# Kernel optimization log

Hardware: AMD Instinct MI355X
Metric: run time of the kernel (lower is better)

## Reference

```python
import jax, jax.numpy as jnp
import numpy as np

N, E, NFEAT, H = 100000, 1600000, 128, 128
NLAYER = 3


def setup_inputs() -> dict:
    key = jax.random.key(0)
    ks = jax.random.split(key, 20)
    s = 0.05
    return {
        "features": jax.random.normal(ks[0], (N, NFEAT), jnp.float32),
        "edge_index": jax.random.randint(ks[1], (2, E), 0, N, jnp.int32),
        "edge_weight": jax.random.uniform(ks[2], (E,), jnp.float32),
        "w1": jax.random.normal(ks[3], (H, NFEAT), jnp.float32) * s,
        "b1": jnp.zeros((H,), jnp.float32),
        "gin_w1": jax.random.normal(ks[4], (NLAYER, H, H), jnp.float32) * s,
        "gin_b1": jnp.zeros((NLAYER, H), jnp.float32),
        "gin_w2": jax.random.normal(ks[5], (NLAYER, H, H), jnp.float32) * s,
        "gin_b2": jnp.zeros((NLAYER, H), jnp.float32),
        "gru_wih": jax.random.normal(ks[6], (NLAYER, 3 * H, H), jnp.float32) * s,
        "gru_whh": jax.random.normal(ks[7], (NLAYER, 3 * H, H), jnp.float32) * s,
        "gru_bih": jnp.zeros((NLAYER, 3 * H), jnp.float32),
        "gru_bhh": jnp.zeros((NLAYER, 3 * H), jnp.float32),
        "head_w1": jax.random.normal(ks[8], (NLAYER, H, H), jnp.float32) * s,
        "head_b1": jnp.zeros((NLAYER, H), jnp.float32),
        "head_w2_0": jax.random.normal(ks[9], (2, H), jnp.float32) * s,
        "head_b2_0": jnp.zeros((2,), jnp.float32),
        "head_w2_1": jax.random.normal(ks[10], (6, H), jnp.float32) * s,
        "head_b2_1": jnp.zeros((6,), jnp.float32),
        "head_w2_2": jax.random.normal(ks[11], (21, H), jnp.float32) * s,
        "head_b2_2": jnp.zeros((21,), jnp.float32),
    }


def _gru_cell(x, h, wih, whh, bih, bhh):
    # torch.nn.GRUCell semantics
    gi = x @ wih.T + bih           # [N, 3H]
    gh = h @ whh.T + bhh           # [N, 3H]
    ir, iz, inn = jnp.split(gi, 3, axis=1)
    hr, hz, hn = jnp.split(gh, 3, axis=1)
    r = jax.nn.sigmoid(ir + hr)
    z = jax.nn.sigmoid(iz + hz)
    n = jnp.tanh(inn + r * hn)
    return (1.0 - z) * n + z * h


def reference(features, edge_index, edge_weight, w1, b1,
              gin_w1, gin_b1, gin_w2, gin_b2,
              gru_wih, gru_whh, gru_bih, gru_bhh,
              head_w1, head_b1,
              head_w2_0, head_b2_0, head_w2_1, head_b2_1, head_w2_2, head_b2_2):
    n_nodes = features.shape[0]
    dst, src = edge_index[0], edge_index[1]  # spmm: out[dst] += w * x[src]
    head_w2 = [head_w2_0, head_w2_1, head_w2_2]
    head_b2 = [head_b2_0, head_b2_1, head_b2_2]

    x = jax.nn.relu(features @ w1.T + b1)  # mlp1 + ReLU
    layer_info = x
    outputs, _outputs = [], []
    for i in range(NLAYER):
        agg = jax.ops.segment_sum(edge_weight[:, None] * x[src], dst,
                                  num_segments=n_nodes)
        h = _gru_cell(agg, layer_info, gru_wih[i], gru_whh[i],
                      gru_bih[i], gru_bhh[i])
        # GinMlp: Linear -> ReLU -> Linear, then outer ReLU
        x = jax.nn.relu(h @ gin_w1[i].T + gin_b1[i]) @ gin_w2[i].T + gin_b2[i]
        x = jax.nn.relu(x)
        # custom layer-norm variant
        x = x / jnp.sqrt(1.0 + jnp.sum(x * x, axis=1, keepdims=True))
        # prediction head for this layer (mlpPos = [0,1,2])
        tmp = jax.nn.relu(x @ head_w1[i].T + head_b1[i]) @ head_w2[i].T + head_b2[i]
        outputs.append(jax.nn.log_softmax(tmp, axis=1))
        _outputs.append(jax.nn.softmax(tmp, axis=1))
        layer_info = x
    return tuple(outputs) + tuple(_outputs)
```

## Files before the change

kernel.cpp:

```cpp
#include <hip/hip_runtime.h>
#include <cstdint>
#include <cstddef>


typedef short  v8s __attribute__((ext_vector_type(8)));
typedef float  v4f __attribute__((ext_vector_type(4)));

#define BUCKET_CAP 4096

static __device__ __forceinline__ float bf2f(uint16_t u) {
  return __uint_as_float(((uint32_t)u) << 16);
}
static __device__ __forceinline__ uint16_t f2b(float f) {
  uint32_t x = __float_as_uint(f);
  return (uint16_t)((x + 0x7FFFu + ((x >> 16) & 1u)) >> 16);
}
static __device__ __forceinline__ float sigmoidf_(float v) {
  return 1.f / (1.f + __expf(-v));
}
static __device__ __forceinline__ float tanhf_(float v) {
  return 1.f - 2.f / (__expf(2.f * v) + 1.f);
}

__global__ void k_detect(const uint32_t* __restrict__ u, int* __restrict__ flag) {
  int lane = threadIdx.x;
  uint32_t low = u[lane] & 0xFFFFu;
  uint32_t e = (low >> 7) & 0xFFu;
  bool pass = (e == 0) || (e >= 110 && e <= 141);
  unsigned long long b = __ballot(pass);
  if (lane == 0) *flag = (__popcll(b) >= 32) ? 1 : 0;
}

struct CvtDesc {
  const void* src[18];
  int off[19];
};

__global__ void k_cvtw(CvtDesc c, float* __restrict__ wbase,
                       uint16_t* __restrict__ wb16,
                       const int* __restrict__ flag, int total) {
  int gid = blockIdx.x * 256 + threadIdx.x;
  if (gid >= total) return;
  int t = 0;
#pragma unroll
  for (int i = 1; i < 18; i++)
    if (gid >= c.off[i]) t = i;
  int local = gid - c.off[t];
  float v;
  if (*flag) v = bf2f(((const uint16_t*)c.src[t])[local]);
  else       v = ((const float*)c.src[t])[local];
  wbase[gid] = v;
  wb16[gid] = f2b(v);
}

__global__ void k_cvt_feat(const void* __restrict__ src, uint16_t* __restrict__ dst,
                           int n, const int* __restrict__ flag) {
  int i = blockIdx.x * 256 + threadIdx.x;
  if (i >= n) return;
  if (*flag) dst[i] = ((const uint16_t*)src)[i];
  else       dst[i] = f2b(((const float*)src)[i]);
}

__global__ void k_zero_i(int* __restrict__ p, int n) {
  int i = blockIdx.x * 256 + threadIdx.x;
  if (i < n) p[i] = 0;
}

__global__ void k_zero_f(float* __restrict__ p, int n) {
  int i = blockIdx.x * 256 + threadIdx.x;
  if (i < n) p[i] = 0.f;
}

__global__ void k_pack_mm(const uint16_t* __restrict__ src, uint16_t* __restrict__ dst,
                          int nmat) {
  int id = blockIdx.x * 256 + threadIdx.x;
  if (id >= nmat * 2048) return;
  int mat = id >> 11;
  int rem = id & 2047;
  int blk = rem >> 6, lane = rem & 63;
  int kc = blk >> 3, t = blk & 7;
  int n0 = lane & 15, quad = lane >> 4;
  const uint16_t* s = src + (size_t)mat * 16384 + (size_t)(t * 16 + n0) * 128 + kc * 32 + quad * 8;
  uint16_t* d = dst + (size_t)id * 8;
  *reinterpret_cast<v8s*>(d) = *reinterpret_cast<const v8s*>(s);
}

__global__ void k_pack_gru(const uint16_t* __restrict__ wih, const uint16_t* __restrict__ whh,
                           uint16_t* __restrict__ dst, int nlayer) {
  int id = blockIdx.x * 256 + threadIdx.x;
  if (id >= nlayer * 192 * 64) return;
  int lane = id & 63;
  int blk = (id >> 6) % 192;
  int layer = (id >> 6) / 192;
  int g = blk % 3;
  int mat = (blk / 3) % 2;
  int u = (blk / 6) % 2;
  int w = (blk / 12) % 4;
  int kc = blk / 48;
  int n0 = lane & 15, quad = lane >> 4;
  const uint16_t* base = (mat == 0 ? wih : whh) + (size_t)layer * 384 * 128;
  const uint16_t* s = base + (size_t)(g * 128 + w * 32 + u * 16 + n0) * 128 + kc * 32 + quad * 8;
  uint16_t* d = dst + ((size_t)layer * 192 + blk) * 512 + (size_t)lane * 8;
  *reinterpret_cast<v8s*>(d) = *reinterpret_cast<const v8s*>(s);
}

__global__ void k_part(const int* __restrict__ dst, const int* __restrict__ src,
                       const void* __restrict__ w, int* __restrict__ gcur,
                       uint2* __restrict__ ep0, const int* __restrict__ flag,
                       int E, int NB) {
  __shared__ int hist[1024];
  __shared__ int lbase[1024];
  int t = threadIdx.x;
  int CH = (E + gridDim.x - 1) / gridDim.x;
  int e0 = blockIdx.x * CH;
  int e1 = e0 + CH;
  if (e1 > E) e1 = E;
  for (int b = t; b < NB; b += 256) hist[b] = 0;
  __syncthreads();
  for (int e = e0 + t; e < e1; e += 256)
    atomicAdd(&hist[dst[e] >> 7], 1);
  __syncthreads();
  for (int b = t; b < NB; b += 256) {
    int c = hist[b];
    lbase[b] = c ? atomicAdd(&gcur[b], c) : 0;
    hist[b] = 0;
  }
  __syncthreads();
  bool bf = (*flag) != 0;
  for (int e = e0 + t; e < e1; e += 256) {
    int d = dst[e];
    int b = d >> 7;
    int pos = lbase[b] + atomicAdd(&hist[b], 1);
    if (pos >= BUCKET_CAP) pos = BUCKET_CAP - 1;
    float wv = bf ? bf2f(((const uint16_t*)w)[e]) : ((const float*)w)[e];
    ep0[(size_t)b * BUCKET_CAP + pos] =
        make_uint2((uint32_t)src[e] | (((uint32_t)d & 127u) << 25),
                   __float_as_uint(wv));
  }
}

__global__ void k_bprefix(const int* __restrict__ gcur, int* __restrict__ bbase,
                          int nbuckets) {
  __shared__ int red[256];
  int t = threadIdx.x;
  int chunk = (nbuckets + 255) >> 8;
  int beg = t * chunk;
  int end = beg + chunk;
  if (end > nbuckets) end = nbuckets;
  int s = 0;
  for (int b = beg; b < end; b++) {
    int c = gcur[b];
    if (c > BUCKET_CAP) c = BUCKET_CAP;
    bbase[b] = c;
    s += c;
  }
  red[t] = s;
  __syncthreads();
  for (int off = 1; off < 256; off <<= 1) {
    int u = (t >= off) ? red[t - off] : 0;
    __syncthreads();
    red[t] += u;
    __syncthreads();
  }
  int run = red[t] - s;
  for (int b = beg; b < end; b++) {
    int tot = bbase[b];
    bbase[b] = run;
    run += tot;
  }
}

__global__ void k_build(const uint2* __restrict__ ep0, const int* __restrict__ gcur,
                        const int* __restrict__ bbase, int* __restrict__ rowptr,
                        uint2* __restrict__ ep, int n, int nbuckets) {
  __shared__ int lcnt[128];
  __shared__ int lsc[128];
  int b = blockIdx.x, t = threadIdx.x;
  int cnt = gcur[b];
  if (cnt > BUCKET_CAP) cnt = BUCKET_CAP;
  if (t < 128) lcnt[t] = 0;
  __syncthreads();

  const uint2* sp = ep0 + (size_t)b * BUCKET_CAP;
  for (int p = t; p < cnt; p += 256)
    atomicAdd(&lcnt[sp[p].x >> 25], 1);
  __syncthreads();

  if (t < 128) lsc[t] = lcnt[t];
  __syncthreads();
  for (int off = 1; off < 128; off <<= 1) {
    int v = 0;
    if (t < 128 && t >= off) v = lsc[t - off];
    __syncthreads();
    if (t < 128) lsc[t] += v;
    __syncthreads();
  }

  int base = bbase[b];
  if (t < 128) {
    int excl = lsc[t] - lcnt[t];
    int node = b * 128 + t;
    if (node < n) rowptr[node] = base + excl;
    lcnt[t] = base + excl;
  }
  if (b == nbuckets - 1 && t == 0) rowptr[n] = base + lsc[127];
  __syncthreads();

  for (int p = t; p < cnt; p += 256) {
    uint2 v = sp[p];
    int pos = atomicAdd(&lcnt[v.x >> 25], 1);
    ep[pos] = make_uint2(v.x & 0x01FFFFFFu, v.y);
  }
}

__global__ void k_spmm(const uint16_t* __restrict__ x, const int* __restrict__ rowptr,
                       const uint2* __restrict__ ep, uint16_t* __restrict__ agg, int n) {
  int node = blockIdx.x * 4 + (threadIdx.x >> 6);
  int lane = threadIdx.x & 63;
  if (node >= n) return;
  int p0 = rowptr[node], p1 = rowptr[node + 1];
  float a0 = 0.f, a1 = 0.f;
  const uint16_t* xc = x + (size_t)lane * 2;
  int p = p0;
  for (; p + 7 < p1; p += 8) {
    uint2 e0 = ep[p], e1 = ep[p + 1], e2 = ep[p + 2], e3 = ep[p + 3];
    uint2 e4 = ep[p + 4], e5 = ep[p + 5], e6 = ep[p + 6], e7 = ep[p + 7];
    uint32_t u0 = *reinterpret_cast<const uint32_t*>(xc + (size_t)e0.x * 128);
    uint32_t u1 = *reinterpret_cast<const uint32_t*>(xc + (size_t)e1.x * 128);
    uint32_t u2 = *reinterpret_cast<const uint32_t*>(xc + (size_t)e2.x * 128);
    uint32_t u3 = *reinterpret_cast<const uint32_t*>(xc + (size_t)e3.x * 128);
    uint32_t u4 = *reinterpret_cast<const uint32_t*>(xc + (size_t)e4.x * 128);
    uint32_t u5 = *reinterpret_cast<const uint32_t*>(xc + (size_t)e5.x * 128);
    uint32_t u6 = *reinterpret_cast<const uint32_t*>(xc + (size_t)e6.x * 128);
    uint32_t u7 = *reinterpret_cast<const uint32_t*>(xc + (size_t)e7.x * 128);
    float w0 = __uint_as_float(e0.y), w1 = __uint_as_float(e1.y);
    float w2 = __uint_as_float(e2.y), w3 = __uint_as_float(e3.y);
    float w4 = __uint_as_float(e4.y), w5 = __uint_as_float(e5.y);
    float w6 = __uint_as_float(e6.y), w7 = __uint_as_float(e7.y);
    a0 = fmaf(w0, bf2f((uint16_t)u0), a0);
    a1 = fmaf(w0, bf2f((uint16_t)(u0 >> 16)), a1);
    a0 = fmaf(w1, bf2f((uint16_t)u1), a0);
    a1 = fmaf(w1, bf2f((uint16_t)(u1 >> 16)), a1);
    a0 = fmaf(w2, bf2f((uint16_t)u2), a0);
    a1 = fmaf(w2, bf2f((uint16_t)(u2 >> 16)), a1);
    a0 = fmaf(w3, bf2f((uint16_t)u3), a0);
    a1 = fmaf(w3, bf2f((uint16_t)(u3 >> 16)), a1);
    a0 = fmaf(w4, bf2f((uint16_t)u4), a0);
    a1 = fmaf(w4, bf2f((uint16_t)(u4 >> 16)), a1);
    a0 = fmaf(w5, bf2f((uint16_t)u5), a0);
    a1 = fmaf(w5, bf2f((uint16_t)(u5 >> 16)), a1);
    a0 = fmaf(w6, bf2f((uint16_t)u6), a0);
    a1 = fmaf(w6, bf2f((uint16_t)(u6 >> 16)), a1);
    a0 = fmaf(w7, bf2f((uint16_t)u7), a0);
    a1 = fmaf(w7, bf2f((uint16_t)(u7 >> 16)), a1);
  }
  for (; p + 1 < p1; p += 2) {
    uint2 e0 = ep[p], e1 = ep[p + 1];
    uint32_t u0 = *reinterpret_cast<const uint32_t*>(xc + (size_t)e0.x * 128);
    uint32_t u1 = *reinterpret_cast<const uint32_t*>(xc + (size_t)e1.x * 128);
    float w0 = __uint_as_float(e0.y), w1 = __uint_as_float(e1.y);
    a0 = fmaf(w0, bf2f((uint16_t)u0), a0);
    a1 = fmaf(w0, bf2f((uint16_t)(u0 >> 16)), a1);
    a0 = fmaf(w1, bf2f((uint16_t)u1), a0);
    a1 = fmaf(w1, bf2f((uint16_t)(u1 >> 16)), a1);
  }
  for (; p < p1; p++) {
    uint2 e0 = ep[p];
    float w0 = __uint_as_float(e0.y);
    uint32_t u0 = *reinterpret_cast<const uint32_t*>(xc + (size_t)e0.x * 128);
    a0 = fmaf(w0, bf2f((uint16_t)u0), a0);
    a1 = fmaf(w0, bf2f((uint16_t)(u0 >> 16)), a1);
  }
  uint32_t packed = (uint32_t)f2b(a0) | ((uint32_t)f2b(a1) << 16);
  *reinterpret_cast<uint32_t*>(agg + (size_t)node * 128 + lane * 2) = packed;
}

template <int EPI>
__launch_bounds__(256)
__global__ void k_mm(const uint16_t* __restrict__ A, const uint16_t* __restrict__ Wrp,
                     const float* __restrict__ bias, uint16_t* __restrict__ C,
                     int nrows) {
  int wave = threadIdx.x >> 6, lane = threadIdx.x & 63;
  int n0 = lane & 15, quad = lane >> 4;
  int m0 = (blockIdx.x * 4 + wave) * 32;
  int r0 = m0 + n0, r1 = m0 + 16 + n0;
  bool ok0 = r0 < nrows, ok1 = r1 < nrows;
  const v8s z8 = {0, 0, 0, 0, 0, 0, 0, 0};

  v4f acc[2][8];
#pragma unroll
  for (int rt = 0; rt < 2; rt++)
#pragma unroll
    for (int t = 0; t < 8; t++) acc[rt][t] = {0.f, 0.f, 0.f, 0.f};

  const uint16_t* ap0 = A + (size_t)r0 * 128 + quad * 8;
  const uint16_t* ap1 = A + (size_t)r1 * 128 + quad * 8;
#pragma unroll
  for (int kc = 0; kc < 4; kc++) {
    v8s a0 = ok0 ? *reinterpret_cast<const v8s*>(ap0 + kc * 32) : z8;
    v8s a1 = ok1 ? *reinterpret_cast<const v8s*>(ap1 + kc * 32) : z8;
    const uint16_t* wp = Wrp + (size_t)kc * 4096 + (size_t)lane * 8;
#pragma unroll
    for (int t = 0; t < 8; t++) {
      v8s bf = *reinterpret_cast<const v8s*>(wp + t * 512);
      acc[0][t] = __builtin_amdgcn_mfma_f32_16x16x32_bf16(a0, bf, acc[0][t], 0, 0, 0);
      acc[1][t] = __builtin_amdgcn_mfma_f32_16x16x32_bf16(a1, bf, acc[1][t], 0, 0, 0);
    }
  }

#pragma unroll
  for (int rt = 0; rt < 2; rt++) {
    int mb = m0 + rt * 16;
    float vv[8][4];
#pragma unroll
    for (int t = 0; t < 8; t++) {
      float b = bias[t * 16 + n0];
#pragma unroll
      for (int r = 0; r < 4; r++) vv[t][r] = fmaxf(acc[rt][t][r] + b, 0.f);
    }
    if (EPI == 2) {
#pragma unroll
      for (int r = 0; r < 4; r++) {
        float ss = 0.f;
#pragma unroll
        for (int t = 0; t < 8; t++) ss = fmaf(vv[t][r], vv[t][r], ss);
        ss += __shfl_xor(ss, 1);
        ss += __shfl_xor(ss, 2);
        ss += __shfl_xor(ss, 4);
        ss += __shfl_xor(ss, 8);
        float sc = rsqrtf(1.f + ss);
#pragma unroll
        for (int t = 0; t < 8; t++) vv[t][r] *= sc;
      }
    }
#pragma unroll
    for (int r = 0; r < 4; r++) {
      int row = mb + quad * 4 + r;
      if (row >= nrows) continue;
#pragma unroll
      for (int t = 0; t < 8; t++)
        C[(size_t)row * 128 + t * 16 + n0] = f2b(vv[t][r]);
    }
  }
}

template <int C>
__launch_bounds__(256)
__global__ void k_mm12h(const uint16_t* __restrict__ A,
                        const uint16_t* __restrict__ W1rp, const float* __restrict__ b1,
                        const uint16_t* __restrict__ W2rp, const float* __restrict__ b2,
                        const uint16_t* __restrict__ Whrp, const float* __restrict__ bh,
                        const float* __restrict__ w2, const float* __restrict__ b2h,
                        uint16_t* __restrict__ xbout,
                        float* __restrict__ out_log, float* __restrict__ out_soft,
                        int nrows) {
  __shared__ uint16_t hl[64][136];
  int wave = threadIdx.x >> 6, lane = threadIdx.x & 63;
  int n0 = lane & 15, quad = lane >> 4;
  int m0 = blockIdx.x * 64 + wave * 16;
  int r0 = m0 + n0;
  bool ok0 = r0 < nrows;
  const v8s z8 = {0, 0, 0, 0, 0, 0, 0, 0};

  v4f acc[8];
#pragma unroll
  for (int t = 0; t < 8; t++) acc[t] = {0.f, 0.f, 0.f, 0.f};

  const uint16_t* ap0 = A + (size_t)r0 * 128 + quad * 8;
#pragma unroll
  for (int kc = 0; kc < 4; kc++) {
    v8s a0 = ok0 ? *reinterpret_cast<const v8s*>(ap0 + kc * 32) : z8;
    const uint16_t* wp = W1rp + (size_t)kc * 4096 + (size_t)lane * 8;
#pragma unroll
    for (int t = 0; t < 8; t++) {
      v8s bf = *reinterpret_cast<const v8s*>(wp + t * 512);
      acc[t] = __builtin_amdgcn_mfma_f32_16x16x32_bf16(a0, bf, acc[t], 0, 0, 0);
    }
  }
#pragma unroll
  for (int t = 0; t < 8; t++) {
    float b = b1[t * 16 + n0];
#pragma unroll
    for (int r = 0; r < 4; r++) {
      int rl = wave * 16 + quad * 4 + r;
      hl[rl][t * 16 + n0] = f2b(fmaxf(acc[t][r] + b, 0.f));
    }
  }
  __syncthreads();

  v4f acc2[8];
#pragma unroll
  for (int t = 0; t < 8; t++) acc2[t] = {0.f, 0.f, 0.f, 0.f};
#pragma unroll
  for (int kc = 0; kc < 4; kc++) {
    v8s a0 = *reinterpret_cast<const v8s*>(&hl[wave * 16 + n0][kc * 32 + quad * 8]);
    const uint16_t* wp = W2rp + (size_t)kc * 4096 + (size_t)lane * 8;
#pragma unroll
    for (int t = 0; t < 8; t++) {
      v8s bf = *reinterpret_cast<const v8s*>(wp + t * 512);
      acc2[t] = __builtin_amdgcn_mfma_f32_16x16x32_bf16(a0, bf, acc2[t], 0, 0, 0);
    }
  }
  __syncthreads();
  {
    float vv[8][4];
#pragma unroll
    for (int t = 0; t < 8; t++) {
      float b = b2[t * 16 + n0];
#pragma unroll
      for (int r = 0; r < 4; r++) vv[t][r] = fmaxf(acc2[t][r] + b, 0.f);
    }
#pragma unroll
    for (int r = 0; r < 4; r++) {
      float ss = 0.f;
#pragma unroll
      for (int t = 0; t < 8; t++) ss = fmaf(vv[t][r], vv[t][r], ss);
      ss += __shfl_xor(ss, 1);
      ss += __shfl_xor(ss, 2);
      ss += __shfl_xor(ss, 4);
      ss += __shfl_xor(ss, 8);
      float sc = rsqrtf(1.f + ss);
#pragma unroll
      for (int t = 0; t < 8; t++) vv[t][r] *= sc;
    }
#pragma unroll
    for (int r = 0; r < 4; r++) {
      int row = m0 + quad * 4 + r;
      int rl = wave * 16 + quad * 4 + r;
#pragma unroll
      for (int t = 0; t < 8; t++) {
        uint16_t hv = f2b(vv[t][r]);
        hl[rl][t * 16 + n0] = hv;
        if (row < nrows) xbout[(size_t)row * 128 + t * 16 + n0] = hv;
      }
    }
  }
  __syncthreads();

  v4f acc3[8];
#pragma unroll
  for (int t = 0; t < 8; t++) acc3[t] = {0.f, 0.f, 0.f, 0.f};
#pragma unroll
  for (int kc = 0; kc < 4; kc++) {
    v8s a0 = *reinterpret_cast<const v8s*>(&hl[wave * 16 + n0][kc * 32 + quad * 8]);
    const uint16_t* wp = Whrp + (size_t)kc * 4096 + (size_t)lane * 8;
#pragma unroll
    for (int t = 0; t < 8; t++) {
      v8s bf = *reinterpret_cast<const v8s*>(wp + t * 512);
      acc3[t] = __builtin_amdgcn_mfma_f32_16x16x32_bf16(a0, bf, acc3[t], 0, 0, 0);
    }
  }
  __syncthreads();
#pragma unroll
  for (int t = 0; t < 8; t++) {
    float b = bh[t * 16 + n0];
#pragma unroll
    for (int r = 0; r < 4; r++) {
      int rl = wave * 16 + quad * 4 + r;
      hl[rl][t * 16 + n0] = f2b(fmaxf(acc3[t][r] + b, 0.f));
    }
  }
  __syncthreads();

  {
    int row = threadIdx.x >> 2;
    int s = threadIdx.x & 3;
    int node = blockIdx.x * 64 + row;
    float lg[C];
#pragma unroll
    for (int c = 0; c < C; c++) lg[c] = 0.f;
    const uint32_t* hr = reinterpret_cast<const uint32_t*>(&hl[row][0]);
#pragma unroll
    for (int j = 0; j < 16; j++) {
      uint32_t u = hr[j * 4 + s];
      float x0 = bf2f((uint16_t)u);
      float x1 = bf2f((uint16_t)(u >> 16));
      int k0 = 2 * (j * 4 + s);
#pragma unroll
      for (int c = 0; c < C; c++) lg[c] = fmaf(x0, w2[c * 128 + k0], lg[c]);
#pragma unroll
      for (int c = 0; c < C; c++) lg[c] = fmaf(x1, w2[c * 128 + k0 + 1], lg[c]);
    }
#pragma unroll
    for (int c = 0; c < C; c++) {
      lg[c] += __shfl_xor(lg[c], 1);
      lg[c] += __shfl_xor(lg[c], 2);
    }
    if (s == 0 && node < nrows) {
#pragma unroll
      for (int c = 0; c < C; c++) lg[c] += b2h[c];
      float m = lg[0];
#pragma unroll
      for (int c = 1; c < C; c++) m = fmaxf(m, lg[c]);
      float sum = 0.f;
      float e[C];
#pragma unroll
      for (int c = 0; c < C; c++) { e[c] = __expf(lg[c] - m); sum += e[c]; }
      float ls = __logf(sum);
      float inv = 1.f / sum;
#pragma unroll
      for (int c = 0; c < C; c++) {
        out_log[(size_t)node * C + c] = lg[c] - m - ls;
        out_soft[(size_t)node * C + c] = e[c] * inv;
      }
    }
  }
}

__launch_bounds__(512, 2)
__global__ void k_gru8(const uint16_t* __restrict__ agg, const uint16_t* __restrict__ xb,
                       const uint16_t* __restrict__ Wrp,
                       const float* __restrict__ bih, const float* __restrict__ bhh,
                       uint16_t* __restrict__ hb, int n, int ntiles) {
  int wave = threadIdx.x >> 6, lane = threadIdx.x & 63;
  int n0 = lane & 15, quad = lane >> 4;
  int s = wave >> 1, u = wave & 1;
  const v8s z8 = {0, 0, 0, 0, 0, 0, 0, 0};

  v8s wf[24];
#pragma unroll
  for (int kc = 0; kc < 4; kc++)
#pragma unroll
    for (int mat = 0; mat < 2; mat++)
#pragma unroll
      for (int g = 0; g < 3; g++)
        wf[kc * 6 + mat * 3 + g] = *reinterpret_cast<const v8s*>(
            Wrp + (size_t)((kc * 4 + s) * 12 + (u * 2 + mat) * 3 + g) * 512 +
            (size_t)lane * 8);

  int col = wave * 16 + n0;
  float bir = bih[col], biz = bih[128 + col], bin = bih[256 + col];
  float bhr = bhh[col], bhz = bhh[128 + col], bhn = bhh[256 + col];

  for (int tt = blockIdx.x; tt < ntiles; tt += gridDim.x) {
    int m0 = tt * 32;
    int r0 = m0 + n0, r1 = m0 + 16 + n0;
    bool ok0 = r0 < n, ok1 = r1 < n;

    v4f accI[2][3], accH[2][3];
#pragma unroll
    for (int rt = 0; rt < 2; rt++)
#pragma unroll
      for (int g = 0; g < 3; g++) {
        accI[rt][g] = {0.f, 0.f, 0.f, 0.f};
        accH[rt][g] = {0.f, 0.f, 0.f, 0.f};
      }

    const uint16_t* ap0 = agg + (size_t)r0 * 128 + quad * 8;
    const uint16_t* ap1 = agg + (size_t)r1 * 128 + quad * 8;
    const uint16_t* xp0 = xb + (size_t)r0 * 128 + quad * 8;
    const uint16_t* xp1 = xb + (size_t)r1 * 128 + quad * 8;
#pragma unroll
    for (int kc = 0; kc < 4; kc++) {
      v8s a0 = ok0 ? *reinterpret_cast<const v8s*>(ap0 + kc * 32) : z8;
      v8s a1 = ok1 ? *reinterpret_cast<const v8s*>(ap1 + kc * 32) : z8;
      v8s x0 = ok0 ? *reinterpret_cast<const v8s*>(xp0 + kc * 32) : z8;
      v8s x1 = ok1 ? *reinterpret_cast<const v8s*>(xp1 + kc * 32) : z8;
#pragma unroll
      for (int g = 0; g < 3; g++) {
        accI[0][g] = __builtin_amdgcn_mfma_f32_16x16x32_bf16(a0, wf[kc * 6 + g], accI[0][g], 0, 0, 0);
        accI[1][g] = __builtin_amdgcn_mfma_f32_16x16x32_bf16(a1, wf[kc * 6 + g], accI[1][g], 0, 0, 0);
        accH[0][g] = __builtin_amdgcn_mfma_f32_16x16x32_bf16(x0, wf[kc * 6 + 3 + g], accH[0][g], 0, 0, 0);
        accH[1][g] = __builtin_amdgcn_mfma_f32_16x16x32_bf16(x1, wf[kc * 6 + 3 + g], accH[1][g], 0, 0, 0);
      }
    }

#pragma unroll
    for (int rt = 0; rt < 2; rt++) {
#pragma unroll
      for (int r = 0; r < 4; r++) {
        int row = m0 + rt * 16 + quad * 4 + r;
        if (row < n) {
          float ir = accI[rt][0][r] + bir;
          float iz = accI[rt][1][r] + biz;
          float in_ = accI[rt][2][r] + bin;
          float hr = accH[rt][0][r] + bhr;
          float hz = accH[rt][1][r] + bhz;
          float hn = accH[rt][2][r] + bhn;
          float rr = sigmoidf_(ir + hr);
          float zz = sigmoidf_(iz + hz);
          float nn = tanhf_(fmaf(rr, hn, in_));
          float xv = bf2f(xb[(size_t)row * 128 + col]);
          hb[(size_t)row * 128 + col] = f2b(fmaf(zz, xv - nn, nn));
        }
      }
    }
  }
}

extern "C" void kernel_launch(void* const* d_in, const int* in_sizes, int n_in,
                              void* d_out, int out_size, void* d_ws, size_t ws_size,
                              hipStream_t stream) {
  const int N = in_sizes[0] / 128;
  const int E = in_sizes[2];
  const int NB = (N + 127) >> 7;

  static const int wn[18] = {16384, 128, 49152, 384, 49152, 384,
                             147456, 147456, 1152, 1152, 49152, 384,
                             256, 2, 768, 6, 2688, 21};
  CvtDesc cd;
  int off = 0;
  for (int i = 0; i < 18; i++) {
    cd.src[i] = d_in[3 + i];
    cd.off[i] = off;
    off += wn[i];
  }
  cd.off[18] = off;
  const int wtotal = off;

  char* p = (char*)d_ws;
  size_t used = 0;
  auto alloc = [&](size_t bytes) -> char* {
    char* r = p;
    size_t b = (bytes + 255) & ~(size_t)255;
    p += b;
    used += b;
    return r;
  };
  int*      flag    = (int*)alloc(256);
  float*    wbase   = (float*)alloc((size_t)wtotal * 4);
  uint16_t* wb16    = (uint16_t*)alloc((size_t)wtotal * 2);
  uint16_t* mmrp    = (uint16_t*)alloc((size_t)10 * 16384 * 2);
  uint16_t* grurp   = (uint16_t*)alloc((size_t)3 * 192 * 512 * 2);
  uint16_t* xb      = (uint16_t*)alloc((size_t)N * 128 * 2);
  uint16_t* aggb    = (uint16_t*)alloc((size_t)N * 128 * 2);
  uint16_t* hb      = (uint16_t*)alloc((size_t)N * 128 * 2);
  int*      rowptr  = (int*)alloc((size_t)(N + 1) * 4);
  int*      gcur    = (int*)alloc((size_t)NB * 4);
  int*      bbase   = (int*)alloc((size_t)(NB + 1) * 4);
  uint2*    ep0     = (uint2*)alloc((size_t)NB * BUCKET_CAP * 8);
  uint2*    epack   = (uint2*)alloc((size_t)E * 8);

  float* out = (float*)d_out;
  float* outlog[3]  = {out, out + 2 * (size_t)N, out + 8 * (size_t)N};
  float* outsoft[3] = {out + 29 * (size_t)N, out + 31 * (size_t)N, out + 37 * (size_t)N};

  if (used > ws_size) {
    k_zero_f<<<(out_size + 255) / 256, 256, 0, stream>>>(out, out_size);
    return;
  }

  float* b1f   = wbase + cd.off[1];
  float* ginb1 = wbase + cd.off[3];
  float* ginb2 = wbase + cd.off[5];
  float* bih   = wbase + cd.off[8];
  float* bhh   = wbase + cd.off[9];
  float* hb1   = wbase + cd.off[11];
  float* hw2_0 = wbase + cd.off[12];
  float* hb2_0 = wbase + cd.off[13];
  float* hw2_1 = wbase + cd.off[14];
  float* hb2_1 = wbase + cd.off[15];
  float* hw2_2 = wbase + cd.off[16];
  float* hb2_2 = wbase + cd.off[17];

  uint16_t* w1b   = wb16 + cd.off[0];
  uint16_t* ginw1b= wb16 + cd.off[2];
  uint16_t* ginw2b= wb16 + cd.off[4];
  uint16_t* wihb  = wb16 + cd.off[6];
  uint16_t* whhb  = wb16 + cd.off[7];
  uint16_t* hw1b  = wb16 + cd.off[10];

  uint16_t* w1rp    = mmrp;
  uint16_t* ginw1rp = mmrp + (size_t)1 * 16384;
  uint16_t* ginw2rp = mmrp + (size_t)4 * 16384;
  uint16_t* hw1rp   = mmrp + (size_t)7 * 16384;

  const int* dst = (const int*)d_in[1];
  const int* src = (const int*)d_in[1] + E;

  k_detect<<<1, 64, 0, stream>>>((const uint32_t*)d_in[0], flag);
  k_cvtw<<<(wtotal + 255) / 256, 256, 0, stream>>>(cd, wbase, wb16, flag, wtotal);
  k_cvt_feat<<<((size_t)N * 128 + 255) / 256, 256, 0, stream>>>(d_in[0], aggb,
                                                                N * 128, flag);
  k_pack_mm<<<(1 * 2048 + 255) / 256, 256, 0, stream>>>(w1b, w1rp, 1);
  k_pack_mm<<<(3 * 2048 + 255) / 256, 256, 0, stream>>>(ginw1b, ginw1rp, 3);
  k_pack_mm<<<(3 * 2048 + 255) / 256, 256, 0, stream>>>(ginw2b, ginw2rp, 3);
  k_pack_mm<<<(3 * 2048 + 255) / 256, 256, 0, stream>>>(hw1b, hw1rp, 3);
  k_pack_gru<<<(3 * 192 * 64 + 255) / 256, 256, 0, stream>>>(wihb, whhb, grurp, 3);

  k_zero_i<<<(NB + 255) / 256, 256, 0, stream>>>(gcur, NB);
  k_part<<<256, 256, 0, stream>>>(dst, src, d_in[2], gcur, ep0, flag, E, NB);
  k_bprefix<<<1, 256, 0, stream>>>(gcur, bbase, NB);
  k_build<<<NB, 256, 0, stream>>>(ep0, gcur, bbase, rowptr, epack, N, NB);

  int mmrb = (N + 127) / 128;
  int mmhb = (N + 63) / 64;
  int spb  = (N + 3) / 4;
  int ntiles32 = (N + 31) / 32;

  k_mm<1><<<mmrb, 256, 0, stream>>>(aggb, w1rp, b1f, xb, N);

  for (int i = 0; i < 3; i++) {
    k_spmm<<<spb, 256, 0, stream>>>(xb, rowptr, epack, aggb, N);
    k_gru8<<<256, 512, 0, stream>>>(aggb, xb, grurp + (size_t)i * 192 * 512,
                                    bih + i * 384, bhh + i * 384, hb, N, ntiles32);
    if (i == 0)
      k_mm12h<2><<<mmhb, 256, 0, stream>>>(hb, ginw1rp + (size_t)i * 16384,
                                           ginb1 + i * 128,
                                           ginw2rp + (size_t)i * 16384,
                                           ginb2 + i * 128,
                                           hw1rp + (size_t)i * 16384, hb1 + i * 128,
                                           hw2_0, hb2_0, xb,
                                           outlog[0], outsoft[0], N);
    else if (i == 1)
      k_mm12h<6><<<mmhb, 256, 0, stream>>>(hb, ginw1rp + (size_t)i * 16384,
                                           ginb1 + i * 128,
                                           ginw2rp + (size_t)i * 16384,
                                           ginb2 + i * 128,
                                           hw1rp + (size_t)i * 16384, hb1 + i * 128,
                                           hw2_1, hb2_1, xb,
                                           outlog[1], outsoft[1], N);
    else
      k_mm12h<21><<<mmhb, 256, 0, stream>>>(hb, ginw1rp + (size_t)i * 16384,
                                            ginb1 + i * 128,
                                            ginw2rp + (size_t)i * 16384,
                                            ginb2 + i * 128,
                                            hw1rp + (size_t)i * 16384, hb1 + i * 128,
                                            hw2_2, hb2_2, xb,
                                            outlog[2], outsoft[2], N);
  }
}
```

Baseline: 869.2 us.

## Retile fused GIN+head kernel to 128-row blocks with per-wave column slices

The fused MLP/head kernel now handles 128 rows per block instead of 64. The input tile is staged into LDS, and each wave owns 32 output columns across all rows. Each wave holds its weight fragments in registers for the whole K loop rather than reloading every weight tile per wave, cutting global weight traffic. The row-norm reduction now crosses waves through a small shared buffer, at the cost of more LDS, an extra barrier and fewer blocks.

```diff
diff --git a/kernel.cpp b/kernel.cpp
--- a/kernel.cpp
+++ b/kernel.cpp
@@ -354,138 +354,187 @@
                         uint16_t* __restrict__ xbout,
                         float* __restrict__ out_log, float* __restrict__ out_soft,
                         int nrows) {
-  __shared__ uint16_t hl[64][136];
+  __shared__ uint16_t hl[128][136];
+  __shared__ float ssq[128][4];
   int wave = threadIdx.x >> 6, lane = threadIdx.x & 63;
   int n0 = lane & 15, quad = lane >> 4;
-  int m0 = blockIdx.x * 64 + wave * 16;
-  int r0 = m0 + n0;
-  bool ok0 = r0 < nrows;
+  int m0 = blockIdx.x * 128;
   const v8s z8 = {0, 0, 0, 0, 0, 0, 0, 0};
 
-  v4f acc[8];
-#pragma unroll
-  for (int t = 0; t < 8; t++) acc[t] = {0.f, 0.f, 0.f, 0.f};
-
-  const uint16_t* ap0 = A + (size_t)r0 * 128 + quad * 8;
-#pragma unroll
-  for (int kc = 0; kc < 4; kc++) {
-    v8s a0 = ok0 ? *reinterpret_cast<const v8s*>(ap0 + kc * 32) : z8;
-    const uint16_t* wp = W1rp + (size_t)kc * 4096 + (size_t)lane * 8;
-#pragma unroll
-    for (int t = 0; t < 8; t++) {
-      v8s bf = *reinterpret_cast<const v8s*>(wp + t * 512);
-      acc[t] = __builtin_amdgcn_mfma_f32_16x16x32_bf16(a0, bf, acc[t], 0, 0, 0);
-    }
-  }
-#pragma unroll
-  for (int t = 0; t < 8; t++) {
-    float b = b1[t * 16 + n0];
+  int col0 = wave * 32 + n0;
+  int col1 = wave * 32 + 16 + n0;
+
+  {
+    int chunk = lane & 15, rsub = lane >> 4;
+#pragma unroll
+    for (int it = 0; it < 8; it++) {
+      int rl = wave * 32 + it * 4 + rsub;
+      int row = m0 + rl;
+      v8s v = (row < nrows)
+            ? *reinterpret_cast<const v8s*>(A + (size_t)row * 128 + chunk * 8) : z8;
+      *reinterpret_cast<v8s*>(&hl[rl][chunk * 8]) = v;
+    }
+  }
+  __syncthreads();
+
+  v4f acc[8][2];
+
+#pragma unroll
+  for (int rt = 0; rt < 8; rt++)
+#pragma unroll
+    for (int u = 0; u < 2; u++) acc[rt][u] = {0.f, 0.f, 0.f, 0.f};
+  {
+    v8s wf[4][2];
+#pragma unroll
+    for (int kc = 0; kc < 4; kc++)
+#pragma unroll
+      for (int u = 0; u < 2; u++)
+        wf[kc][u] = *reinterpret_cast<const v8s*>(
+            W1rp + (size_t)kc * 4096 + (size_t)(wave * 2 + u) * 512 + (size_t)lane * 8);
+#pragma unroll
+    for (int kc = 0; kc < 4; kc++) {
+#pragma unroll
+      for (int rt = 0; rt < 8; rt++) {
+        v8s a = *reinterpret_cast<const v8s*>(&hl[rt * 16 + n0][kc * 32 + quad * 8]);
+        acc[rt][0] = __builtin_amdgcn_mfma_f32_16x16x32_bf16(a, wf[kc][0], acc[rt][0], 0, 0, 0);
+        acc[rt][1] = __builtin_amdgcn_mfma_f32_16x16x32_bf16(a, wf[kc][1], acc[rt][1], 0, 0, 0);
+      }
+    }
+  }
+  __syncthreads();
+  {
+    float bb0 = b1[col0], bb1 = b1[col1];
+#pragma unroll
+    for (int rt = 0; rt < 8; rt++)
+#pragma unroll
+      for (int r = 0; r < 4; r++) {
+        int rl = rt * 16 + quad * 4 + r;
+        hl[rl][col0] = f2b(fmaxf(acc[rt][0][r] + bb0, 0.f));
+        hl[rl][col1] = f2b(fmaxf(acc[rt][1][r] + bb1, 0.f));
+      }
+  }
+  __syncthreads();
+
+#pragma unroll
+  for (int rt = 0; rt < 8; rt++)
+#pragma unroll
+    for (int u = 0; u < 2; u++) acc[rt][u] = {0.f, 0.f, 0.f, 0.f};
+  {
+    v8s wf[4][2];
+#pragma unroll
+    for (int kc = 0; kc < 4; kc++)
+#pragma unroll
+      for (int u = 0; u < 2; u++)
+        wf[kc][u] = *reinterpret_cast<const v8s*>(
+            W2rp + (size_t)kc * 4096 + (size_t)(wave * 2 + u) * 512 + (size_t)lane * 8);
+#pragma unroll
+    for (int kc = 0; kc < 4; kc++) {
+#pragma unroll
+      for (int rt = 0; rt < 8; rt++) {
+        v8s a = *reinterpret_cast<const v8s*>(&hl[rt * 16 + n0][kc * 32 + quad * 8]);
+        acc[rt][0] = __builtin_amdgcn_mfma_f32_16x16x32_bf16(a, wf[kc][0], acc[rt][0], 0, 0, 0);
+        acc[rt][1] = __builtin_amdgcn_mfma_f32_16x16x32_bf16(a, wf[kc][1], acc[rt][1], 0, 0, 0);
+      }
+    }
+  }
+  __syncthreads();
+  {
+    float bb0 = b2[col0], bb1 = b2[col1];
+#pragma unroll
+    for (int rt = 0; rt < 8; rt++) {
+#pragma unroll
+      for (int r = 0; r < 4; r++) {
+        float v0 = fmaxf(acc[rt][0][r] + bb0, 0.f);
+        float v1 = fmaxf(acc[rt][1][r] + bb1, 0.f);
+        acc[rt][0][r] = v0;
+        acc[rt][1][r] = v1;
+        float ss = fmaf(v0, v0, v1 * v1);
+        ss += __shfl_xor(ss, 1);
+        ss += __shfl_xor(ss, 2);
+        ss += __shfl_xor(ss, 4);
+        ss += __shfl_xor(ss, 8);
+        if (n0 == 0) ssq[rt * 16 + quad * 4 + r][wave] = ss;
+      }
+    }
+  }
+  __syncthreads();
+#pragma unroll
+  for (int rt = 0; rt < 8; rt++) {
 #pragma unroll
     for (int r = 0; r < 4; r++) {
-      int rl = wave * 16 + quad * 4 + r;
-      hl[rl][t * 16 + n0] = f2b(fmaxf(acc[t][r] + b, 0.f));
-    }
-  }
-  __syncthreads();
-
-  v4f acc2[8];
-#pragma unroll
-  for (int t = 0; t < 8; t++) acc2[t] = {0.f, 0.f, 0.f, 0.f};
-#pragma unroll
-  for (int kc = 0; kc < 4; kc++) {
-    v8s a0 = *reinterpret_cast<const v8s*>(&hl[wave * 16 + n0][kc * 32 + quad * 8]);
-    const uint16_t* wp = W2rp + (size_t)kc * 4096 + (size_t)lane * 8;
-#pragma unroll
-    for (int t = 0; t < 8; t++) {
-      v8s bf = *reinterpret_cast<const v8s*>(wp + t * 512);
-      acc2[t] = __builtin_amdgcn_mfma_f32_16x16x32_bf16(a0, bf, acc2[t], 0, 0, 0);
-    }
-  }
-  __syncthreads();
+      int rl = rt * 16 + quad * 4 + r;
+      float s4 = ssq[rl][0] + ssq[rl][1] + ssq[rl][2] + ssq[rl][3];
+      float sc = rsqrtf(1.f + s4);
+      uint16_t h0 = f2b(acc[rt][0][r] * sc);
+      uint16_t h1 = f2b(acc[rt][1][r] * sc);
+      hl[rl][col0] = h0;
+      hl[rl][col1] = h1;
+      int row = m0 + rl;
+      if (row < nrows) {
+        xbout[(size_t)row * 128 + col0] = h0;
+        xbout[(size_t)row * 128 + col1] = h1;
+      }
+    }
+  }
+  __syncthreads();
+
+#pragma unroll
+  for (int rt = 0; rt < 8; rt++)
+#pragma unroll
+    for (int u = 0; u < 2; u++) acc[rt][u] = {0.f, 0.f, 0.f, 0.f};
   {
-    float vv[8][4];
-#pragma unroll
-    for (int t = 0; t < 8; t++) {
-      float b = b2[t * 16 + n0];
-#pragma unroll
-      for (int r = 0; r < 4; r++) vv[t][r] = fmaxf(acc2[t][r] + b, 0.f);
-    }
-#pragma unroll
-    for (int r = 0; r < 4; r++) {
-      float ss = 0.f;
-#pragma unroll
-      for (int t = 0; t < 8; t++) ss = fmaf(vv[t][r], vv[t][r], ss);
-      ss += __shfl_xor(ss, 1);
-      ss += __shfl_xor(ss, 2);
-      ss += __shfl_xor(ss, 4);
-      ss += __shfl_xor(ss, 8);
-      float sc = rsqrtf(1.f + ss);
-#pragma unroll
-      for (int t = 0; t < 8; t++) vv[t][r] *= sc;
-    }
-#pragma unroll
-    for (int r = 0; r < 4; r++) {
-      int row = m0 + quad * 4 + r;
-      int rl = wave * 16 + quad * 4 + r;
-#pragma unroll
-      for (int t = 0; t < 8; t++) {
-        uint16_t hv = f2b(vv[t][r]);
-        hl[rl][t * 16 + n0] = hv;
-        if (row < nrows) xbout[(size_t)row * 128 + t * 16 + n0] = hv;
-      }
-    }
-  }
-  __syncthreads();
-
-  v4f acc3[8];
-#pragma unroll
-  for (int t = 0; t < 8; t++) acc3[t] = {0.f, 0.f, 0.f, 0.f};
-#pragma unroll
-  for (int kc = 0; kc < 4; kc++) {
-    v8s a0 = *reinterpret_cast<const v8s*>(&hl[wave * 16 + n0][kc * 32 + quad * 8]);
-    const uint16_t* wp = Whrp + (size_t)kc * 4096 + (size_t)lane * 8;
-#pragma unroll
-    for (int t = 0; t < 8; t++) {
-      v8s bf = *reinterpret_cast<const v8s*>(wp + t * 512);
-      acc3[t] = __builtin_amdgcn_mfma_f32_16x16x32_bf16(a0, bf, acc3[t], 0, 0, 0);
-    }
-  }
-  __syncthreads();
-#pragma unroll
-  for (int t = 0; t < 8; t++) {
-    float b = bh[t * 16 + n0];
-#pragma unroll
-    for (int r = 0; r < 4; r++) {
-      int rl = wave * 16 + quad * 4 + r;
-      hl[rl][t * 16 + n0] = f2b(fmaxf(acc3[t][r] + b, 0.f));
-    }
-  }
-  __syncthreads();
-
+    v8s wf[4][2];
+#pragma unroll
+    for (int kc = 0; kc < 4; kc++)
+#pragma unroll
+      for (int u = 0; u < 2; u++)
+        wf[kc][u] = *reinterpret_cast<const v8s*>(
+            Whrp + (size_t)kc * 4096 + (size_t)(wave * 2 + u) * 512 + (size_t)lane * 8);
+#pragma unroll
+    for (int kc = 0; kc < 4; kc++) {
+#pragma unroll
+      for (int rt = 0; rt < 8; rt++) {
+        v8s a = *reinterpret_cast<const v8s*>(&hl[rt * 16 + n0][kc * 32 + quad * 8]);
+        acc[rt][0] = __builtin_amdgcn_mfma_f32_16x16x32_bf16(a, wf[kc][0], acc[rt][0], 0, 0, 0);
+        acc[rt][1] = __builtin_amdgcn_mfma_f32_16x16x32_bf16(a, wf[kc][1], acc[rt][1], 0, 0, 0);
+      }
+    }
+  }
+  __syncthreads();
   {
-    int row = threadIdx.x >> 2;
-    int s = threadIdx.x & 3;
-    int node = blockIdx.x * 64 + row;
+    float bb0 = bh[col0], bb1 = bh[col1];
+#pragma unroll
+    for (int rt = 0; rt < 8; rt++)
+#pragma unroll
+      for (int r = 0; r < 4; r++) {
+        int rl = rt * 16 + quad * 4 + r;
+        hl[rl][col0] = f2b(fmaxf(acc[rt][0][r] + bb0, 0.f));
+        hl[rl][col1] = f2b(fmaxf(acc[rt][1][r] + bb1, 0.f));
+      }
+  }
+  __syncthreads();
+
+  {
+    int row = threadIdx.x >> 1;
+    int s = threadIdx.x & 1;
+    int node = m0 + row;
     float lg[C];
 #pragma unroll
     for (int c = 0; c < C; c++) lg[c] = 0.f;
     const uint32_t* hr = reinterpret_cast<const uint32_t*>(&hl[row][0]);
 #pragma unroll
-    for (int j = 0; j < 16; j++) {
-      uint32_t u = hr[j * 4 + s];
+    for (int j = 0; j < 32; j++) {
+      uint32_t u = hr[j * 2 + s];
       float x0 = bf2f((uint16_t)u);
       float x1 = bf2f((uint16_t)(u >> 16));
-      int k0 = 2 * (j * 4 + s);
+      int k0 = 2 * (j * 2 + s);
 #pragma unroll
       for (int c = 0; c < C; c++) lg[c] = fmaf(x0, w2[c * 128 + k0], lg[c]);
 #pragma unroll
       for (int c = 0; c < C; c++) lg[c] = fmaf(x1, w2[c * 128 + k0 + 1], lg[c]);
     }
 #pragma unroll
-    for (int c = 0; c < C; c++) {
-      lg[c] += __shfl_xor(lg[c], 1);
-      lg[c] += __shfl_xor(lg[c], 2);
-    }
+    for (int c = 0; c < C; c++) lg[c] += __shfl_xor(lg[c], 1);
     if (s == 0 && node < nrows) {
 #pragma unroll
       for (int c = 0; c < C; c++) lg[c] += b2h[c];
@@ -684,7 +733,6 @@
   k_build<<<NB, 256, 0, stream>>>(ep0, gcur, bbase, rowptr, epack, N, NB);
 
   int mmrb = (N + 127) / 128;
-  int mmhb = (N + 63) / 64;
   int spb  = (N + 3) / 4;
   int ntiles32 = (N + 31) / 32;
 
@@ -695,7 +743,7 @@
     k_gru8<<<256, 512, 0, stream>>>(aggb, xb, grurp + (size_t)i * 192 * 512,
                                     bih + i * 384, bhh + i * 384, hb, N, ntiles32);
     if (i == 0)
-      k_mm12h<2><<<mmhb, 256, 0, stream>>>(hb, ginw1rp + (size_t)i * 16384,
+      k_mm12h<2><<<mmrb, 256, 0, stream>>>(hb, ginw1rp + (size_t)i * 16384,
                                            ginb1 + i * 128,
                                            ginw2rp + (size_t)i * 16384,
                                            ginb2 + i * 128,
@@ -703,7 +751,7 @@
                                            hw2_0, hb2_0, xb,
                                            outlog[0], outsoft[0], N);
     else if (i == 1)
-      k_mm12h<6><<<mmhb, 256, 0, stream>>>(hb, ginw1rp + (size_t)i * 16384,
+      k_mm12h<6><<<mmrb, 256, 0, stream>>>(hb, ginw1rp + (size_t)i * 16384,
                                            ginb1 + i * 128,
                                            ginw2rp + (size_t)i * 16384,
                                            ginb2 + i * 128,
@@ -711,7 +759,7 @@
                                            hw2_1, hb2_1, xb,
                                            outlog[1], outsoft[1], N);
     else
-      k_mm12h<21><<<mmhb, 256, 0, stream>>>(hb, ginw1rp + (size_t)i * 16384,
+      k_mm12h<21><<<mmrb, 256, 0, stream>>>(hb, ginw1rp + (size_t)i * 16384,
                                             ginb1 + i * 128,
                                             ginw2rp + (size_t)i * 16384,
                                             ginb2 + i * 128,
```

Result: no change. 878.8 us (+1.1%).
